# Optimization experiments

Hardware: AMD Instinct MI355X
Metric: run time of the kernel (lower is better)

The kernel has to match this reference:

```python
import jax, jax.numpy as jnp
import numpy as np

B, N, D, S, ITERS = 64, 2048, 256, 8, 3
SCALE = D ** -0.5
EPS_LN = 1e-5

def _ln(x, g, b):
    m = jnp.mean(x, axis=-1, keepdims=True)
    v = jnp.var(x, axis=-1, keepdims=True)
    return (x - m) / jnp.sqrt(v + EPS_LN) * g + b

def setup_inputs() -> dict:
    key = jax.random.key(0)
    ks = jax.random.split(key, 20)
    s = D ** -0.5
    f32 = jnp.float32
    return dict(
        x=jax.random.normal(ks[0], (B, N, D), f32),
        noise=jax.random.normal(ks[1], (B, S, D), f32),
        slots_mu=jax.random.normal(ks[2], (1, 1, D), f32),
        slots_sigma=jax.random.normal(ks[3], (1, 1, D), f32),
        Wq=jax.random.normal(ks[4], (D, D), f32) * s, bq=jnp.zeros((D,), f32),
        Wk=jax.random.normal(ks[5], (D, D), f32) * s, bk=jnp.zeros((D,), f32),
        Wv=jax.random.normal(ks[6], (D, D), f32) * s, bv=jnp.zeros((D,), f32),
        W_ih=jax.random.normal(ks[7], (3 * D, D), f32) * s, b_ih=jnp.zeros((3 * D,), f32),
        W_hh=jax.random.normal(ks[8], (3 * D, D), f32) * s, b_hh=jnp.zeros((3 * D,), f32),
        W1=jax.random.normal(ks[9], (D, D), f32) * s, b1=jnp.zeros((D,), f32),
        W2=jax.random.normal(ks[10], (D, D), f32) * s, b2=jnp.zeros((D,), f32),
        g_in=jnp.ones((D,), f32), be_in=jnp.zeros((D,), f32),
        g_sl=jnp.ones((D,), f32), be_sl=jnp.zeros((D,), f32),
        g_ff=jnp.ones((D,), f32), be_ff=jnp.zeros((D,), f32),
    )

def reference(x, noise, slots_mu, slots_sigma, Wq, bq, Wk, bk, Wv, bv,
              W_ih, b_ih, W_hh, b_hh, W1, b1, W2, b2,
              g_in, be_in, g_sl, be_sl, g_ff, be_ff):
    # slot init: mu + softplus(sigma) * noise  -> [B,S,D]
    slots = slots_mu + jax.nn.softplus(slots_sigma) * noise
    xn = _ln(x, g_in, be_in)
    k = xn @ Wk.T + bk  # [B,N,D]
    v = xn @ Wv.T + bv
    for _ in range(ITERS):
        prev = slots
        q = _ln(slots, g_sl, be_sl) @ Wq.T + bq  # [B,S,D]
        logits = jnp.einsum('bsd,bnd->bsn', q, k) * SCALE
        attn = jax.nn.softmax(logits, axis=-1) + 1e-8  # softmax over inputs, as in source
        attn = attn / jnp.sum(attn, axis=-1, keepdims=True)
        updates = jnp.einsum('bsn,bnd->bsd', attn, v)
        # GRUCell(input=updates, hidden=prev); torch gate order r,z,n
        gi = updates @ W_ih.T + b_ih
        gh = prev @ W_hh.T + b_hh
        ir, iz, i_n = jnp.split(gi, 3, axis=-1)
        hr, hz, h_n = jnp.split(gh, 3, axis=-1)
        r = jax.nn.sigmoid(ir + hr)
        z = jax.nn.sigmoid(iz + hz)
        n = jnp.tanh(i_n + r * h_n)
        slots = (1.0 - z) * n + z * prev
        # residual MLP
        h = jax.nn.relu(_ln(slots, g_ff, be_ff) @ W1.T + b1)
        slots = slots + (h @ W2.T + b2)
    return slots
```

## Files before the change

### kernel.cpp

```cpp
#include <hip/hip_runtime.h>
#include <cstddef>


#define BB 64
#define NN 2048
#define DD 256
#define NCH 32
#define CHK 64
#define NITER 3
#define XPITCH 264

typedef unsigned short u16;
typedef unsigned int u32;
typedef _Float16 h2 __attribute__((ext_vector_type(2)));
typedef _Float16 h4 __attribute__((ext_vector_type(4)));

#if defined(__has_builtin)
#if __has_builtin(__builtin_amdgcn_fdot2)
#define HAS_FDOT2 1
#endif
#endif

#ifdef HAS_FDOT2
#define FDOT2(a,b,c) __builtin_amdgcn_fdot2((a),(b),(c),false)
#else
#define FDOT2(a,b,c) fmaf((float)(a).y,(float)(b).y, fmaf((float)(a).x,(float)(b).x,(c)))
#endif

__device__ __forceinline__ h2 u2h2(u32 v){ union{u32 u; h2 h;} c; c.u=v; return c.h; }
__device__ __forceinline__ float u16f(u16 v){ union{u16 u; _Float16 h;} c; c.u=v; return (float)c.h; }

__global__ __launch_bounds__(256) void kA(const float* __restrict__ noise, const float* __restrict__ mu,
                                          const float* __restrict__ sig, float* __restrict__ S,
                                          const float* __restrict__ Wq, const float* __restrict__ Wk,
                                          const float* __restrict__ bq, const float* __restrict__ Wih,
                                          const float* __restrict__ Wv, const float* __restrict__ bv,
                                          const float* __restrict__ bih,
                                          float* __restrict__ Wqk, float* __restrict__ bqk,
                                          float* __restrict__ Wihv, float* __restrict__ bihv){
  __shared__ float col[256];
  const int t = threadIdx.x;
  const int blk = blockIdx.x;
  if(blk < 256){
    col[t] = Wq[t*256 + blk];
    __syncthreads();
    float acc = 0.f;
    #pragma unroll 4
    for(int j=0;j<256;j++) acc += col[j]*Wk[j*256+t];
    Wqk[blk*256+t] = acc * 0.0625f;
  } else if(blk < 1024){
    int c = blk - 256;
    col[t] = Wih[c*256+t];
    __syncthreads();
    float acc = 0.f;
    #pragma unroll 4
    for(int j=0;j<256;j++) acc += col[j]*Wv[j*256+t];
    Wihv[(size_t)c*256+t] = acc;
  } else if(blk < 1536){
    int i = (blk-1024)*256 + t;
    float sg = sig[t];
    float sp = fmaxf(sg, 0.f) + log1pf(expf(-fabsf(sg)));
    S[i] = mu[t] + sp * noise[i];
  } else if(blk == 1536){
    float acc = 0.f;
    for(int j=0;j<256;j++) acc += bq[j]*Wk[j*256+t];
    bqk[t] = acc * 0.0625f;
  } else {
    for(int c=t;c<768;c+=256){
      float acc = 0.f;
      for(int j=0;j<256;j++) acc += Wih[c*256+j]*bv[j];
      bihv[c] = acc + bih[c];
    }
  }
}

__global__ __launch_bounds__(256) void kB(const float* __restrict__ Wihv, const float* __restrict__ Whh,
                                          const float* __restrict__ W1, const float* __restrict__ W2,
                                          float* __restrict__ WihvT, float* __restrict__ WhhT,
                                          float* __restrict__ W1T, float* __restrict__ W2T,
                                          const float* __restrict__ S0, const float* __restrict__ g_sl,
                                          const float* __restrict__ be_sl, const float* __restrict__ Wqk,
                                          const float* __restrict__ bqk, float* __restrict__ Qq){
  __shared__ float tile[64][65];
  __shared__ float lnA[8][256];
  const int blk = blockIdx.x, t = threadIdx.x;
  if(blk < 128){
    const float* src; float* dst; int R, C, tb;
    if(blk < 48){ src=Wihv; dst=WihvT; R=768; C=256; tb=blk; }
    else if(blk < 96){ src=Whh; dst=WhhT; R=768; C=256; tb=blk-48; }
    else if(blk < 112){ src=W1; dst=W1T; R=256; C=256; tb=blk-96; }
    else { src=W2; dst=W2T; R=256; C=256; tb=blk-112; }
    const int tilesC = C/64;
    const int r0 = (tb/tilesC)*64, c0 = (tb%tilesC)*64;
    const int x = t&63, y = t>>6;
    #pragma unroll
    for(int k=0;k<16;k++) tile[y*16+k][x] = src[(size_t)(r0+y*16+k)*C + c0+x];
    __syncthreads();
    #pragma unroll
    for(int k=0;k<16;k++) dst[(size_t)(c0+y*16+k)*R + r0+x] = tile[x][y*16+k];
    return;
  }
  const int w = t>>6, l = t&63;
  const int r0 = (blk-128)*8;
  #pragma unroll
  for(int rr=0; rr<2; rr++){
    int r = w*2 + rr;
    float4 v = *(const float4*)(S0 + (size_t)(r0+r)*256 + l*4);
    float s1 = v.x+v.y+v.z+v.w;
    float s2 = v.x*v.x+v.y*v.y+v.z*v.z+v.w*v.w;
    #pragma unroll
    for(int off=1; off<64; off<<=1){ s1 += __shfl_xor(s1,off); s2 += __shfl_xor(s2,off); }
    float m = s1*(1.f/256.f);
    float var = s2*(1.f/256.f) - m*m;
    float rs = rsqrtf(var + 1e-5f);
    float4 gg = *(const float4*)(g_sl + l*4);
    float4 bb = *(const float4*)(be_sl + l*4);
    float4 o;
    o.x=(v.x-m)*rs*gg.x+bb.x; o.y=(v.y-m)*rs*gg.y+bb.y;
    o.z=(v.z-m)*rs*gg.z+bb.z; o.w=(v.w-m)*rs*gg.w+bb.w;
    *(float4*)(&lnA[r][l*4]) = o;
  }
  __syncthreads();
  const int c4 = l*4;
  float acc[2][4] = {};
  #pragma unroll 2
  for(int k=0;k<256;k++){
    float4 wv = *(const float4*)(Wqk + (size_t)k*256 + c4);
    float a0 = lnA[2*w][k], a1 = lnA[2*w+1][k];
    acc[0][0]+=a0*wv.x; acc[0][1]+=a0*wv.y; acc[0][2]+=a0*wv.z; acc[0][3]+=a0*wv.w;
    acc[1][0]+=a1*wv.x; acc[1][1]+=a1*wv.y; acc[1][2]+=a1*wv.z; acc[1][3]+=a1*wv.w;
  }
  float4 bq4 = *(const float4*)(bqk + c4);
  #pragma unroll
  for(int rr=0; rr<2; rr++){
    float4 o;
    o.x=acc[rr][0]+bq4.x; o.y=acc[rr][1]+bq4.y; o.z=acc[rr][2]+bq4.z; o.w=acc[rr][3]+bq4.w;
    *(float4*)(Qq + (size_t)(r0+2*w+rr)*256 + c4) = o;
  }
}

template<int ITER0>
__global__ __launch_bounds__(512) void k_attnP(const float* __restrict__ x, const float* __restrict__ g_in,
                                               const float* __restrict__ be_in, u16* __restrict__ xn,
                                               const float* __restrict__ Qq,
                                               float* __restrict__ mP, float* __restrict__ lP,
                                               u16* __restrict__ aPh){
  __shared__ __align__(16) u16 xs[CHK*XPITCH];
  __shared__ h2 qs[8][128];
  __shared__ float plT[8][64];
  __shared__ float mS[8], lS[8];
  const int g = blockIdx.x, t = threadIdx.x;
  const int b = g & 63, c0 = g >> 6;
  const int w = t>>6, l = t&63;

  for(int i=t; i<1024; i+=512){
    int s = i>>7, p = i&127;
    h2 hv;
    hv.x = (_Float16)Qq[b*2048 + s*256 + 2*p];
    hv.y = (_Float16)Qq[b*2048 + s*256 + 2*p + 1];
    qs[s][p] = hv;
  }
  float4 gg, bb;
  if(ITER0){ gg = *(const float4*)(g_in + l*4); bb = *(const float4*)(be_in + l*4); }

  float4 pf[ITER0 ? 8 : 4];

  {
    const int c = c0;
    if(ITER0){
      const float* xb = x + ((size_t)b*NN + (size_t)c*CHK)*DD;
      #pragma unroll
      for(int j=0;j<8;j++)
        pf[j] = *(const float4*)(xb + (size_t)(w+8*j)*256 + l*4);
    } else {
      const uint4* xg4 = (const uint4*)(xn + ((size_t)b*NN + (size_t)c*CHK)*DD);
      #pragma unroll
      for(int k=0;k<4;k++)
        *(uint4*)&pf[k] = xg4[t + 512*k];
    }
  }

  #pragma unroll
  for(int i=0;i<4;i++){
    const int c = c0 + 8*i;
    if(ITER0){
      const size_t rowbase = (size_t)b*NN + (size_t)c*CHK;
      #pragma unroll
      for(int j=0;j<8;j++){
        int row = w + 8*j;
        float4 v = pf[j];
        float s1 = v.x+v.y+v.z+v.w;
        float s2 = v.x*v.x + v.y*v.y + v.z*v.z + v.w*v.w;
        #pragma unroll
        for(int off=1; off<64; off<<=1){ s1 += __shfl_xor(s1,off); s2 += __shfl_xor(s2,off); }
        float m = s1*(1.f/256.f);
        float var = s2*(1.f/256.f) - m*m;
        float rs = rsqrtf(var + 1e-5f);
        union { h4 h; uint2 u2v; } pk;
        pk.h[0] = (_Float16)((v.x-m)*rs*gg.x + bb.x);
        pk.h[1] = (_Float16)((v.y-m)*rs*gg.y + bb.y);
        pk.h[2] = (_Float16)((v.z-m)*rs*gg.z + bb.z);
        pk.h[3] = (_Float16)((v.w-m)*rs*gg.w + bb.w);
        *(uint2*)(xs + (size_t)row*XPITCH + l*4) = pk.u2v;
        *(uint2*)(xn + (rowbase+row)*DD + l*4) = pk.u2v;
      }
    } else {
      #pragma unroll
      for(int k=0;k<4;k++){
        int idx = t + 512*k;
        int n = idx>>5, j = idx&31;
        *(uint4*)(xs + (size_t)n*XPITCH + j*8) = *(uint4*)&pf[k];
      }
    }
    __syncthreads();

    if(i < 3){
      const int cn = c0 + 8*(i+1);
      if(ITER0){
        const float* xb = x + ((size_t)b*NN + (size_t)cn*CHK)*DD;
        #pragma unroll
        for(int j=0;j<8;j++)
          pf[j] = *(const float4*)(xb + (size_t)(w+8*j)*256 + l*4);
      } else {
        const uint4* xg4 = (const uint4*)(xn + ((size_t)b*NN + (size_t)cn*CHK)*DD);
        #pragma unroll
        for(int k=0;k<4;k++)
          *(uint4*)&pf[k] = xg4[t + 512*k];
      }
    }

    float lg = 0.f;
    {
      const u16* xr = xs + (size_t)l*XPITCH;
      #pragma unroll 4
      for(int d8=0; d8<32; ++d8){
        uint4 u = *(const uint4*)(xr + d8*8);
        h2 xa=u2h2(u.x), xb2=u2h2(u.y), xc=u2h2(u.z), xd=u2h2(u.w);
        const h2* qp = &qs[w][d8*4];
        lg = FDOT2(xa, qp[0], lg);
        lg = FDOT2(xb2, qp[1], lg);
        lg = FDOT2(xc, qp[2], lg);
        lg = FDOT2(xd, qp[3], lg);
      }
    }
    float mx = lg;
    #pragma unroll
    for(int off=1; off<64; off<<=1) mx = fmaxf(mx, __shfl_xor(mx, off));
    float p = __expf(lg - mx);
    float sm = p;
    #pragma unroll
    for(int off=1; off<64; off<<=1) sm += __shfl_xor(sm, off);
    plT[w][l] = p;
    if(l==0){ mS[w] = mx; lS[w] = sm; }
    __syncthreads();

    const size_t pb = (size_t)(b*NCH + c)*8;
    {
      float4 a4 = {0.f,0.f,0.f,0.f};
      const u16* xq = xs + 4*l;
      #pragma unroll 8
      for(int nn=0; nn<64; ++nn){
        uint2 u = *(const uint2*)(xq + (size_t)nn*XPITCH);
        h2 ha=u2h2(u.x), hb=u2h2(u.y);
        float pp = plT[w][nn];
        a4.x += pp*(float)ha.x; a4.y += pp*(float)ha.y;
        a4.z += pp*(float)hb.x; a4.w += pp*(float)hb.y;
      }
      union { h4 h; uint2 u2v; } pk;
      pk.h[0]=(_Float16)a4.x; pk.h[1]=(_Float16)a4.y;
      pk.h[2]=(_Float16)a4.z; pk.h[3]=(_Float16)a4.w;
      *(uint2*)(aPh + (pb + w)*256 + l*4) = pk.u2v;
    }
    if(t<8){ mP[pb+t] = mS[t]; lP[pb+t] = lS[t]; }
    __syncthreads();
  }
}

union PostU {
  float Gt[2][4][768];
  struct { float Row[4][256]; float Ht[4][256]; float Lq[4][256]; } m;
};

__global__ __launch_bounds__(512) void k_post(const float* __restrict__ mP, const float* __restrict__ lP,
                                              const u16* __restrict__ aPh, const float* __restrict__ WihvT,
                                              const float* __restrict__ bihv, const float* __restrict__ WhhT,
                                              const float* __restrict__ bhh, const float* __restrict__ Sc,
                                              const float* __restrict__ g_ff, const float* __restrict__ be_ff,
                                              const float* __restrict__ W1T, const float* __restrict__ b1,
                                              const float* __restrict__ W2T, const float* __restrict__ b2,
                                              const float* __restrict__ g_sl, const float* __restrict__ be_sl,
                                              const float* __restrict__ Wqk, const float* __restrict__ bqk,
                                              float* __restrict__ Sout, float* __restrict__ Qq, int writeQ){
  __shared__ float Ut[4][256];
  __shared__ float Sp[4][256];
  __shared__ float Hp[2][4][256];
  __shared__ PostU uu;
  __shared__ float red2[4][2];
  const int t = threadIdx.x;
  const int r0 = blockIdx.x*4;
  const int b = r0>>3;
  const int w = t>>6, l = t&63;
  const int c = t&255, hh = t>>8;

  #pragma unroll
  for(int k=0;k<2;k++){
    int idx = t + 512*k;
    int r = idx>>8, cc = idx&255;
    int rr = r0 + r, ss = rr&7;
    const float* mpb = mP + b*(NCH*8) + ss;
    const float* lpb = lP + b*(NCH*8) + ss;
    float M = -1e30f;
    #pragma unroll
    for(int c8=0;c8<NCH;c8++) M = fmaxf(M, mpb[c8*8]);
    float L = 0.f;
    float wc[NCH];
    #pragma unroll
    for(int c8=0;c8<NCH;c8++){ wc[c8] = __expf(mpb[c8*8] - M); L += lpb[c8*8]*wc[c8]; }
    float inv = 1.f/L;
    size_t base = ((size_t)b*(NCH*8) + ss)*256 + cc;
    float u = 0.f;
    #pragma unroll
    for(int c8=0;c8<NCH;c8++) u += wc[c8]*u16f(aPh[base + (size_t)c8*2048]);
    Ut[r][cc] = u*inv;
    Sp[r][cc] = Sc[(size_t)rr*256 + cc];
  }
  __syncthreads();

  if(t < 384){
    const int mat = t/192, q4 = (t - mat*192)*4;
    const float* WT = mat ? WhhT : WihvT;
    const float* bb2 = mat ? bhh : bihv;
    const float (*A)[256] = mat ? Sp : Ut;
    float4 bias4 = *(const float4*)(bb2 + q4);
    float4 ac0 = bias4, ac1 = bias4, ac2 = bias4, ac3 = bias4;
    const float* wp = WT + q4;
    #pragma unroll 4
    for(int d=0; d<256; ++d){
      float4 wv = *(const float4*)(wp + (size_t)d*768);
      float a0=A[0][d], a1=A[1][d], a2=A[2][d], a3=A[3][d];
      ac0.x += a0*wv.x; ac0.y += a0*wv.y; ac0.z += a0*wv.z; ac0.w += a0*wv.w;
      ac1.x += a1*wv.x; ac1.y += a1*wv.y; ac1.z += a1*wv.z; ac1.w += a1*wv.w;
      ac2.x += a2*wv.x; ac2.y += a2*wv.y; ac2.z += a2*wv.z; ac2.w += a2*wv.w;
      ac3.x += a3*wv.x; ac3.y += a3*wv.y; ac3.z += a3*wv.z; ac3.w += a3*wv.w;
    }
    *(float4*)(&uu.Gt[mat][0][q4]) = ac0;
    *(float4*)(&uu.Gt[mat][1][q4]) = ac1;
    *(float4*)(&uu.Gt[mat][2][q4]) = ac2;
    *(float4*)(&uu.Gt[mat][3][q4]) = ac3;
  }
  __syncthreads();

  #pragma unroll
  for(int k=0;k<2;k++){
    int idx = t + 512*k;
    int r = idx>>8, cc = idx&255;
    float gir = uu.Gt[0][r][cc], giz = uu.Gt[0][r][256+cc], gin = uu.Gt[0][r][512+cc];
    float ghr = uu.Gt[1][r][cc], ghz = uu.Gt[1][r][256+cc], ghn = uu.Gt[1][r][512+cc];
    float rr2 = 1.f/(1.f + __expf(-(gir+ghr)));
    float zz = 1.f/(1.f + __expf(-(giz+ghz)));
    float nn = tanhf(gin + rr2*ghn);
    Ut[r][cc] = (1.f-zz)*nn + zz*Sp[r][cc];
  }
  __syncthreads();

  if(w < 4){
    float s1=0.f, s2=0.f;
    #pragma unroll
    for(int k2=0;k2<4;k2++){ float v = Ut[w][l + 64*k2]; s1 += v; s2 += v*v; }
    #pragma unroll
    for(int off=1; off<64; off<<=1){ s1 += __shfl_xor(s1,off); s2 += __shfl_xor(s2,off); }
    if(l==0){
      float m = s1*(1.f/256.f);
      float var = s2*(1.f/256.f) - m*m;
      red2[w][0] = m; red2[w][1] = rsqrtf(var + 1e-5f);
    }
  }
  __syncthreads();
  #pragma unroll
  for(int k=0;k<2;k++){
    int idx = t + 512*k;
    int r = idx>>8, cc = idx&255;
    uu.m.Row[r][cc] = (Ut[r][cc]-red2[r][0])*red2[r][1]*g_ff[cc] + be_ff[cc];
  }
  __syncthreads();

  {
    const float* w1 = W1T + (size_t)hh*128*256 + c;
    float a0 = hh ? 0.f : b1[c], a1=a0, a2=a0, a3=a0;
    const int dB = hh*128;
    #pragma unroll 8
    for(int d=0; d<128; ++d){
      float wv = w1[(size_t)d*256];
      a0 += uu.m.Row[0][dB+d]*wv;
      a1 += uu.m.Row[1][dB+d]*wv;
      a2 += uu.m.Row[2][dB+d]*wv;
      a3 += uu.m.Row[3][dB+d]*wv;
    }
    Hp[hh][0][c]=a0; Hp[hh][1][c]=a1; Hp[hh][2][c]=a2; Hp[hh][3][c]=a3;
  }
  __syncthreads();
  #pragma unroll
  for(int k=0;k<2;k++){
    int idx = t + 512*k;
    int r = idx>>8, cc = idx&255;
    uu.m.Ht[r][cc] = fmaxf(Hp[0][r][cc]+Hp[1][r][cc], 0.f);
  }
  __syncthreads();

  {
    const float* w2 = W2T + (size_t)hh*128*256 + c;
    float a0 = hh ? 0.f : b2[c], a1=a0, a2=a0, a3=a0;
    const int dB = hh*128;
    #pragma unroll 8
    for(int d=0; d<128; ++d){
      float wv = w2[(size_t)d*256];
      a0 += uu.m.Ht[0][dB+d]*wv;
      a1 += uu.m.Ht[1][dB+d]*wv;
      a2 += uu.m.Ht[2][dB+d]*wv;
      a3 += uu.m.Ht[3][dB+d]*wv;
    }
    Hp[hh][0][c]=a0; Hp[hh][1][c]=a1; Hp[hh][2][c]=a2; Hp[hh][3][c]=a3;
  }
  __syncthreads();
  if(t < 256){
    #pragma unroll
    for(int r=0;r<4;r++){
      float sn = Hp[0][r][c] + Hp[1][r][c] + Ut[r][c];
      Sout[(size_t)(r0+r)*256 + c] = sn;
      Ut[r][c] = sn;
    }
  }

  if(writeQ){
    __syncthreads();
    if(w < 4){
      float s1=0.f, s2=0.f;
      #pragma unroll
      for(int k2=0;k2<4;k2++){ float v = Ut[w][l + 64*k2]; s1 += v; s2 += v*v; }
      #pragma unroll
      for(int off=1; off<64; off<<=1){ s1 += __shfl_xor(s1,off); s2 += __shfl_xor(s2,off); }
      if(l==0){
        float m = s1*(1.f/256.f);
        float var = s2*(1.f/256.f) - m*m;
        red2[w][0] = m; red2[w][1] = rsqrtf(var + 1e-5f);
      }
    }
    __syncthreads();
    #pragma unroll
    for(int k=0;k<2;k++){
      int idx = t + 512*k;
      int r = idx>>8, cc = idx&255;
      uu.m.Lq[r][cc] = (Ut[r][cc]-red2[r][0])*red2[r][1]*g_sl[cc] + be_sl[cc];
    }
    __syncthreads();
    {
      const float* wq = Wqk + (size_t)hh*128*256 + c;
      float a0 = hh ? 0.f : bqk[c], a1=a0, a2=a0, a3=a0;
      const int dB = hh*128;
      #pragma unroll 8
      for(int d=0; d<128; ++d){
        float wv = wq[(size_t)d*256];
        a0 += uu.m.Lq[0][dB+d]*wv;
        a1 += uu.m.Lq[1][dB+d]*wv;
        a2 += uu.m.Lq[2][dB+d]*wv;
        a3 += uu.m.Lq[3][dB+d]*wv;
      }
      Hp[hh][0][c]=a0; Hp[hh][1][c]=a1; Hp[hh][2][c]=a2; Hp[hh][3][c]=a3;
    }
    __syncthreads();
    if(t < 256){
      #pragma unroll
      for(int r=0;r<4;r++)
        Qq[(size_t)(r0+r)*256 + c] = Hp[0][r][c] + Hp[1][r][c];
    }
  }
}

extern "C" void kernel_launch(void* const* d_in, const int* in_sizes, int n_in,
                              void* d_out, int out_size, void* d_ws, size_t ws_size,
                              hipStream_t stream){
  const float* x    = (const float*)d_in[0];
  const float* noise= (const float*)d_in[1];
  const float* mu   = (const float*)d_in[2];
  const float* sig  = (const float*)d_in[3];
  const float* Wq   = (const float*)d_in[4];
  const float* bq   = (const float*)d_in[5];
  const float* Wk   = (const float*)d_in[6];
  const float* Wv   = (const float*)d_in[8];
  const float* bv   = (const float*)d_in[9];
  const float* W_ih = (const float*)d_in[10];
  const float* b_ih = (const float*)d_in[11];
  const float* W_hh = (const float*)d_in[12];
  const float* b_hh = (const float*)d_in[13];
  const float* W1m  = (const float*)d_in[14];
  const float* b1v  = (const float*)d_in[15];
  const float* W2m  = (const float*)d_in[16];
  const float* b2v  = (const float*)d_in[17];
  const float* g_in = (const float*)d_in[18];
  const float* be_in= (const float*)d_in[19];
  const float* g_sl = (const float*)d_in[20];
  const float* be_sl= (const float*)d_in[21];
  const float* g_ff = (const float*)d_in[22];
  const float* be_ff= (const float*)d_in[23];

  char* p = (char*)d_ws;
  auto alloc = [&](size_t bytes)->char*{ char* q = p; p += (bytes + 255) & ~(size_t)255; return q; };
  u16*   xn    = (u16*)  alloc((size_t)BB*NN*DD*2);
  float* Wqk   = (float*)alloc(256*256*4);
  float* bqk   = (float*)alloc(256*4);
  float* Wihv  = (float*)alloc((size_t)768*256*4);
  float* WihvT = (float*)alloc((size_t)256*768*4);
  float* bihv  = (float*)alloc(768*4);
  float* WhhT  = (float*)alloc((size_t)256*768*4);
  float* W1T   = (float*)alloc(256*256*4);
  float* W2T   = (float*)alloc(256*256*4);
  float* S0    = (float*)alloc(512*256*4);
  float* S1    = (float*)alloc(512*256*4);
  float* Qq    = (float*)alloc(512*256*4);
  float* mP    = (float*)alloc(64*NCH*8*4);
  float* lP    = (float*)alloc(64*NCH*8*4);
  u16*   aPh   = (u16*)  alloc((size_t)64*NCH*8*256*2);
  if((size_t)(p - (char*)d_ws) > ws_size) return;

  kA<<<1538, 256, 0, stream>>>(noise, mu, sig, S0, Wq, Wk, bq, W_ih, Wv, bv, b_ih,
                               Wqk, bqk, Wihv, bihv);
  kB<<<192, 256, 0, stream>>>(Wihv, W_hh, W1m, W2m, WihvT, WhhT, W1T, W2T,
                              S0, g_sl, be_sl, Wqk, bqk, Qq);

  float* Sin = S0;
  float* Sping[2] = { S1, S0 };
  for(int it=0; it<NITER; ++it){
    float* Sout = (it==NITER-1) ? (float*)d_out : Sping[it&1];
    if(it == 0)
      k_attnP<1><<<512, 512, 0, stream>>>(x, g_in, be_in, xn, Qq, mP, lP, aPh);
    else
      k_attnP<0><<<512, 512, 0, stream>>>(x, g_in, be_in, xn, Qq, mP, lP, aPh);
    k_post<<<128, 512, 0, stream>>>(mP, lP, aPh, WihvT, bihv, WhhT, b_hh, Sin, g_ff, be_ff,
                                    W1T, b1v, W2T, b2v, g_sl, be_sl, Wqk, bqk,
                                    Sout, Qq, (it<NITER-1) ? 1 : 0);
    Sin = Sout;
  }
}
```

Measured before the change: 343.9 us.

## Shrink attention chunks to 32 rows and launch one block per chunk

The chunk size drops from 64 to 32 rows and the number of chunks rises from 32 to 64. The attention kernel now launches a 64x64 grid with one chunk per block, replacing 512 blocks that each looped over 4 chunks with register prefetch. In the logit pass, two half-waves split the D dimension and combine their partial dot products with a shuffle. The post kernel's chunk merge now streams in a single loop instead of holding a 32-entry register array. The goal is more blocks and better latency hiding, at the cost of twice as many partial results to write and merge, repeated Q loads per block, and the loss of the software prefetch.

```diff
diff --git a/kernel.cpp b/kernel.cpp
--- a/kernel.cpp
+++ b/kernel.cpp
@@ -5,8 +5,8 @@
 #define BB 64
 #define NN 2048
 #define DD 256
-#define NCH 32
-#define CHK 64
+#define NCH 64
+#define CHK 32
 #define NITER 3
 #define XPITCH 264
 
@@ -147,12 +147,44 @@
                                                u16* __restrict__ aPh){
   __shared__ __align__(16) u16 xs[CHK*XPITCH];
   __shared__ h2 qs[8][128];
-  __shared__ float plT[8][64];
+  __shared__ float plT[8][32];
   __shared__ float mS[8], lS[8];
-  const int g = blockIdx.x, t = threadIdx.x;
-  const int b = g & 63, c0 = g >> 6;
+  const int b = blockIdx.x, c = blockIdx.y, t = threadIdx.x;
   const int w = t>>6, l = t&63;
 
+  if(ITER0){
+    const size_t rowbase = (size_t)b*NN + (size_t)c*CHK;
+    const float* xb = x + rowbase*DD;
+    float4 gg = *(const float4*)(g_in + l*4);
+    float4 bb = *(const float4*)(be_in + l*4);
+    #pragma unroll
+    for(int k=0;k<4;k++){
+      int row = w + 8*k;
+      float4 v = *(const float4*)(xb + (size_t)row*256 + l*4);
+      float s1 = v.x+v.y+v.z+v.w;
+      float s2 = v.x*v.x + v.y*v.y + v.z*v.z + v.w*v.w;
+      #pragma unroll
+      for(int off=1; off<64; off<<=1){ s1 += __shfl_xor(s1,off); s2 += __shfl_xor(s2,off); }
+      float m = s1*(1.f/256.f);
+      float var = s2*(1.f/256.f) - m*m;
+      float rs = rsqrtf(var + 1e-5f);
+      union { h4 h; uint2 u2v; } pk;
+      pk.h[0] = (_Float16)((v.x-m)*rs*gg.x + bb.x);
+      pk.h[1] = (_Float16)((v.y-m)*rs*gg.y + bb.y);
+      pk.h[2] = (_Float16)((v.z-m)*rs*gg.z + bb.z);
+      pk.h[3] = (_Float16)((v.w-m)*rs*gg.w + bb.w);
+      *(uint2*)(xs + (size_t)row*XPITCH + l*4) = pk.u2v;
+      *(uint2*)(xn + (rowbase+row)*DD + l*4) = pk.u2v;
+    }
+  } else {
+    const uint4* xg4 = (const uint4*)(xn + ((size_t)b*NN + (size_t)c*CHK)*DD);
+    #pragma unroll
+    for(int k=0;k<2;k++){
+      int idx = t + 512*k;
+      int n = idx>>5, j = idx&31;
+      *(uint4*)(xs + (size_t)n*XPITCH + j*8) = xg4[idx];
+    }
+  }
   for(int i=t; i<1024; i+=512){
     int s = i>>7, p = i&127;
     h2 hv;
@@ -160,120 +192,54 @@
     hv.y = (_Float16)Qq[b*2048 + s*256 + 2*p + 1];
     qs[s][p] = hv;
   }
-  float4 gg, bb;
-  if(ITER0){ gg = *(const float4*)(g_in + l*4); bb = *(const float4*)(be_in + l*4); }
-
-  float4 pf[ITER0 ? 8 : 4];
-
+  __syncthreads();
+
+  const int r = l & 31, hf = l >> 5;
+  float hd = 0.f;
   {
-    const int c = c0;
-    if(ITER0){
-      const float* xb = x + ((size_t)b*NN + (size_t)c*CHK)*DD;
-      #pragma unroll
-      for(int j=0;j<8;j++)
-        pf[j] = *(const float4*)(xb + (size_t)(w+8*j)*256 + l*4);
-    } else {
-      const uint4* xg4 = (const uint4*)(xn + ((size_t)b*NN + (size_t)c*CHK)*DD);
-      #pragma unroll
-      for(int k=0;k<4;k++)
-        *(uint4*)&pf[k] = xg4[t + 512*k];
-    }
-  }
-
-  #pragma unroll
-  for(int i=0;i<4;i++){
-    const int c = c0 + 8*i;
-    if(ITER0){
-      const size_t rowbase = (size_t)b*NN + (size_t)c*CHK;
-      #pragma unroll
-      for(int j=0;j<8;j++){
-        int row = w + 8*j;
-        float4 v = pf[j];
-        float s1 = v.x+v.y+v.z+v.w;
-        float s2 = v.x*v.x + v.y*v.y + v.z*v.z + v.w*v.w;
-        #pragma unroll
-        for(int off=1; off<64; off<<=1){ s1 += __shfl_xor(s1,off); s2 += __shfl_xor(s2,off); }
-        float m = s1*(1.f/256.f);
-        float var = s2*(1.f/256.f) - m*m;
-        float rs = rsqrtf(var + 1e-5f);
-        union { h4 h; uint2 u2v; } pk;
-        pk.h[0] = (_Float16)((v.x-m)*rs*gg.x + bb.x);
-        pk.h[1] = (_Float16)((v.y-m)*rs*gg.y + bb.y);
-        pk.h[2] = (_Float16)((v.z-m)*rs*gg.z + bb.z);
-        pk.h[3] = (_Float16)((v.w-m)*rs*gg.w + bb.w);
-        *(uint2*)(xs + (size_t)row*XPITCH + l*4) = pk.u2v;
-        *(uint2*)(xn + (rowbase+row)*DD + l*4) = pk.u2v;
-      }
-    } else {
-      #pragma unroll
-      for(int k=0;k<4;k++){
-        int idx = t + 512*k;
-        int n = idx>>5, j = idx&31;
-        *(uint4*)(xs + (size_t)n*XPITCH + j*8) = *(uint4*)&pf[k];
-      }
-    }
-    __syncthreads();
-
-    if(i < 3){
-      const int cn = c0 + 8*(i+1);
-      if(ITER0){
-        const float* xb = x + ((size_t)b*NN + (size_t)cn*CHK)*DD;
-        #pragma unroll
-        for(int j=0;j<8;j++)
-          pf[j] = *(const float4*)(xb + (size_t)(w+8*j)*256 + l*4);
-      } else {
-        const uint4* xg4 = (const uint4*)(xn + ((size_t)b*NN + (size_t)cn*CHK)*DD);
-        #pragma unroll
-        for(int k=0;k<4;k++)
-          *(uint4*)&pf[k] = xg4[t + 512*k];
-      }
-    }
-
-    float lg = 0.f;
-    {
-      const u16* xr = xs + (size_t)l*XPITCH;
-      #pragma unroll 4
-      for(int d8=0; d8<32; ++d8){
-        uint4 u = *(const uint4*)(xr + d8*8);
-        h2 xa=u2h2(u.x), xb2=u2h2(u.y), xc=u2h2(u.z), xd=u2h2(u.w);
-        const h2* qp = &qs[w][d8*4];
-        lg = FDOT2(xa, qp[0], lg);
-        lg = FDOT2(xb2, qp[1], lg);
-        lg = FDOT2(xc, qp[2], lg);
-        lg = FDOT2(xd, qp[3], lg);
-      }
-    }
-    float mx = lg;
-    #pragma unroll
-    for(int off=1; off<64; off<<=1) mx = fmaxf(mx, __shfl_xor(mx, off));
-    float p = __expf(lg - mx);
-    float sm = p;
-    #pragma unroll
-    for(int off=1; off<64; off<<=1) sm += __shfl_xor(sm, off);
-    plT[w][l] = p;
-    if(l==0){ mS[w] = mx; lS[w] = sm; }
-    __syncthreads();
-
-    const size_t pb = (size_t)(b*NCH + c)*8;
-    {
-      float4 a4 = {0.f,0.f,0.f,0.f};
-      const u16* xq = xs + 4*l;
-      #pragma unroll 8
-      for(int nn=0; nn<64; ++nn){
-        uint2 u = *(const uint2*)(xq + (size_t)nn*XPITCH);
-        h2 ha=u2h2(u.x), hb=u2h2(u.y);
-        float pp = plT[w][nn];
-        a4.x += pp*(float)ha.x; a4.y += pp*(float)ha.y;
-        a4.z += pp*(float)hb.x; a4.w += pp*(float)hb.y;
-      }
-      union { h4 h; uint2 u2v; } pk;
-      pk.h[0]=(_Float16)a4.x; pk.h[1]=(_Float16)a4.y;
-      pk.h[2]=(_Float16)a4.z; pk.h[3]=(_Float16)a4.w;
-      *(uint2*)(aPh + (pb + w)*256 + l*4) = pk.u2v;
-    }
-    if(t<8){ mP[pb+t] = mS[t]; lP[pb+t] = lS[t]; }
-    __syncthreads();
-  }
+    const u16* xr = xs + (size_t)r*XPITCH + hf*128;
+    const h2* qp0 = &qs[w][hf*64];
+    #pragma unroll
+    for(int d8=0; d8<16; ++d8){
+      uint4 u = *(const uint4*)(xr + d8*8);
+      h2 xa=u2h2(u.x), xb2=u2h2(u.y), xc=u2h2(u.z), xd=u2h2(u.w);
+      const h2* qp = qp0 + d8*4;
+      hd = FDOT2(xa, qp[0], hd);
+      hd = FDOT2(xb2, qp[1], hd);
+      hd = FDOT2(xc, qp[2], hd);
+      hd = FDOT2(xd, qp[3], hd);
+    }
+  }
+  float lg = hd + __shfl_xor(hd, 32);
+  float mx = lg;
+  #pragma unroll
+  for(int off=1; off<32; off<<=1) mx = fmaxf(mx, __shfl_xor(mx, off));
+  float p = __expf(lg - mx);
+  float sm = p;
+  #pragma unroll
+  for(int off=1; off<32; off<<=1) sm += __shfl_xor(sm, off);
+  if(l < 32) plT[w][r] = p;
+  if(l == 0){ mS[w] = mx; lS[w] = sm; }
+  __syncthreads();
+
+  const size_t pb = (size_t)(b*NCH + c)*8;
+  {
+    float4 a4 = {0.f,0.f,0.f,0.f};
+    const u16* xq = xs + 4*l;
+    #pragma unroll 8
+    for(int nn=0; nn<CHK; ++nn){
+      uint2 u = *(const uint2*)(xq + (size_t)nn*XPITCH);
+      h2 ha=u2h2(u.x), hb=u2h2(u.y);
+      float pp = plT[w][nn];
+      a4.x += pp*(float)ha.x; a4.y += pp*(float)ha.y;
+      a4.z += pp*(float)hb.x; a4.w += pp*(float)hb.y;
+    }
+    union { h4 h; uint2 u2v; } pk;
+    pk.h[0]=(_Float16)a4.x; pk.h[1]=(_Float16)a4.y;
+    pk.h[2]=(_Float16)a4.z; pk.h[3]=(_Float16)a4.w;
+    *(uint2*)(aPh + (pb + w)*256 + l*4) = pk.u2v;
+  }
+  if(t<8){ mP[pb+t] = mS[t]; lP[pb+t] = lS[t]; }
 }
 
 union PostU {
@@ -310,18 +276,17 @@
     const float* mpb = mP + b*(NCH*8) + ss;
     const float* lpb = lP + b*(NCH*8) + ss;
     float M = -1e30f;
-    #pragma unroll
+    #pragma unroll 8
     for(int c8=0;c8<NCH;c8++) M = fmaxf(M, mpb[c8*8]);
-    float L = 0.f;
-    float wc[NCH];
-    #pragma unroll
-    for(int c8=0;c8<NCH;c8++){ wc[c8] = __expf(mpb[c8*8] - M); L += lpb[c8*8]*wc[c8]; }
-    float inv = 1.f/L;
+    float L = 0.f, u = 0.f;
     size_t base = ((size_t)b*(NCH*8) + ss)*256 + cc;
-    float u = 0.f;
-    #pragma unroll
-    for(int c8=0;c8<NCH;c8++) u += wc[c8]*u16f(aPh[base + (size_t)c8*2048]);
-    Ut[r][cc] = u*inv;
+    #pragma unroll 8
+    for(int c8=0;c8<NCH;c8++){
+      float wgt = __expf(mpb[c8*8] - M);
+      L += lpb[c8*8]*wgt;
+      u += wgt*u16f(aPh[base + (size_t)c8*2048]);
+    }
+    Ut[r][cc] = u/L;
     Sp[r][cc] = Sc[(size_t)rr*256 + cc];
   }
   __syncthreads();
@@ -532,9 +497,9 @@
   for(int it=0; it<NITER; ++it){
     float* Sout = (it==NITER-1) ? (float*)d_out : Sping[it&1];
     if(it == 0)
-      k_attnP<1><<<512, 512, 0, stream>>>(x, g_in, be_in, xn, Qq, mP, lP, aPh);
+      k_attnP<1><<<dim3(64, NCH), 512, 0, stream>>>(x, g_in, be_in, xn, Qq, mP, lP, aPh);
     else
-      k_attnP<0><<<512, 512, 0, stream>>>(x, g_in, be_in, xn, Qq, mP, lP, aPh);
+      k_attnP<0><<<dim3(64, NCH), 512, 0, stream>>>(x, g_in, be_in, xn, Qq, mP, lP, aPh);
     k_post<<<128, 512, 0, stream>>>(mP, lP, aPh, WihvT, bihv, WhhT, b_hh, Sin, g_ff, be_ff,
                                     W1T, b1v, W2T, b2v, g_sl, be_sl, Wqk, bqk,
                                     Sout, Qq, (it<NITER-1) ? 1 : 0);
```

Result: slower. 363.2 us (+5.6%).
